# Performance work log

Measured on AMD Instinct MI355X. Metric: run time of the kernel, lower is better.

Reference implementation:

```python
import jax, jax.numpy as jnp
import numpy as np

N_NODES = 100000
N_EDGES = 1000000
D = 64
HID = 64
OUT = 64
N_CLS = 10
N_GRAPHS = 512
BN_EPS = 1e-5


def setup_inputs() -> dict:
    key = jax.random.key(0)
    ks = jax.random.split(key, 16)
    inp = {
        "x": jax.random.normal(ks[0], (N_NODES, D), dtype=jnp.float32),
        "edge_index": jax.random.randint(ks[1], (2, N_EDGES), 0, N_NODES, dtype=jnp.int32),
        "batch": jnp.sort(jax.random.randint(ks[2], (N_NODES,), 0, N_GRAPHS, dtype=jnp.int32)),
    }
    def lin(k, fi, fo):
        lim = 1.0 / np.sqrt(fi)
        kw, kb = jax.random.split(k)
        return (jax.random.uniform(kw, (fi, fo), minval=-lim, maxval=lim, dtype=jnp.float32),
                jax.random.uniform(kb, (fo,), minval=-lim, maxval=lim, dtype=jnp.float32))
    # conv0 MLP([64,64,64]) with BN after first linear
    inp["w0a"], inp["b0a"] = lin(ks[3], D, HID)
    inp["g0"] = jnp.ones((HID,), jnp.float32); inp["be0"] = jnp.zeros((HID,), jnp.float32)
    inp["m0"] = jnp.zeros((HID,), jnp.float32); inp["v0"] = jnp.ones((HID,), jnp.float32)
    inp["w0b"], inp["b0b"] = lin(ks[4], HID, HID)
    # conv1 MLP([64,64,64])
    inp["w1a"], inp["b1a"] = lin(ks[5], HID, HID)
    inp["g1"] = jnp.ones((HID,), jnp.float32); inp["be1"] = jnp.zeros((HID,), jnp.float32)
    inp["m1"] = jnp.zeros((HID,), jnp.float32); inp["v1"] = jnp.ones((HID,), jnp.float32)
    inp["w1b"], inp["b1b"] = lin(ks[6], HID, OUT)
    # classifier
    inp["wc"], inp["bc"] = lin(ks[7], OUT, N_CLS)
    return inp


def _bn_eval(h, g, b, m, v):
    return (h - m) * jax.lax.rsqrt(v + BN_EPS) * g + b


def _mlp(h, wa, ba, g, be, m, v, wb, bb):
    # Linear -> BN -> ReLU -> (dropout eval=identity) -> Linear
    h = h @ wa + ba
    h = jax.nn.relu(_bn_eval(h, g, be, m, v))
    return h @ wb + bb


def _gin_conv(h, src, dst, wa, ba, g, be, m, v, wb, bb):
    # GINConv eps=0: mlp(x + sum_{j->i} x_j), messages scatter-added at dst
    agg = jax.ops.segment_sum(h[src], dst, num_segments=N_NODES)
    return _mlp(h + agg, wa, ba, g, be, m, v, wb, bb)


def reference(x, edge_index, batch,
              w0a, b0a, g0, be0, m0, v0, w0b, b0b,
              w1a, b1a, g1, be1, m1, v1, w1b, b1b,
              wc, bc):
    src, dst = edge_index[0], edge_index[1]
    h = _gin_conv(x, src, dst, w0a, b0a, g0, be0, m0, v0, w0b, b0b)
    h = jax.nn.relu(h)  # dropout is identity in eval
    h = _gin_conv(h, src, dst, w1a, b1a, g1, be1, m1, v1, w1b, b1b)
    # global mean pool over batch indices
    sums = jax.ops.segment_sum(h, batch, num_segments=N_GRAPHS)
    cnts = jax.ops.segment_sum(jnp.ones((h.shape[0],), h.dtype), batch, num_segments=N_GRAPHS)
    pooled = sums / jnp.maximum(cnts, 1.0)[:, None]
    return pooled @ wc + bc
```

## Files before the change

### kernel.cpp

```cpp
#include <hip/hip_runtime.h>

#define N_NODES 100000
#define N_EDGES 1000000
#define N_GRAPHS 512
#define N_CLS 10
#define BN_EPS 1e-5f

#define SCAN_NB 200
#define NTILES2 3125

typedef _Float16 half8 __attribute__((ext_vector_type(8)));
typedef _Float16 half4v __attribute__((ext_vector_type(4)));
typedef float floatx4 __attribute__((ext_vector_type(4)));

__global__ __launch_bounds__(256) void prep_kernel(
    const float* __restrict__ x, _Float16* __restrict__ xh,
    const int* __restrict__ batch, const int* __restrict__ dstI,
    int* __restrict__ deg, int* __restrict__ rank,
    const float* __restrict__ w0a, const float* __restrict__ b0a,
    const float* __restrict__ g0, const float* __restrict__ be0,
    const float* __restrict__ m0, const float* __restrict__ v0,
    const float* __restrict__ w0b,
    const float* __restrict__ w1a, const float* __restrict__ b1a,
    const float* __restrict__ g1, const float* __restrict__ be1,
    const float* __restrict__ m1, const float* __restrict__ v1,
    const float* __restrict__ w1b,
    int* __restrict__ gstart,
    _Float16* __restrict__ wHi, _Float16* __restrict__ wLo,
    float* __restrict__ b1p0, float* __restrict__ b1p1) {
    const int gid = blockIdx.x * 256 + threadIdx.x;

    if (gid < 1600000) {
        float4 v = ((const float4*)x)[gid];
        half4v h = {(_Float16)v.x, (_Float16)v.y, (_Float16)v.z, (_Float16)v.w};
        ((half4v*)xh)[gid] = h;
    }

    if (gid < N_EDGES)
        rank[gid] = atomicAdd(&deg[dstI[gid]], 1);

    if (gid <= N_NODES) {
        int bcur = (gid < N_NODES) ? batch[gid] : N_GRAPHS;
        int bprev = (gid > 0) ? batch[gid - 1] : -1;
        for (int g = bprev + 1; g <= bcur; ++g) gstart[g] = gid;
    }

    if (gid < 16384) {
        const int e = gid & 4095, mat = gid >> 12;
        const int jj = e & 7, lane = (e >> 3) & 63, c = (e >> 9) & 3, k0 = (e >> 11) & 1;
        const int k = k0 * 32 + (lane >> 4) * 8 + jj;
        const int col = c * 16 + (lane & 15);
        float val;
        if (mat == 0)      val = w0a[k * 64 + col] * (rsqrtf(v0[col] + BN_EPS) * g0[col]);
        else if (mat == 1) val = w0b[k * 64 + col];
        else if (mat == 2) val = w1a[k * 64 + col] * (rsqrtf(v1[col] + BN_EPS) * g1[col]);
        else               val = w1b[k * 64 + col];
        _Float16 hi = (_Float16)val;
        wHi[gid] = hi;
        wLo[gid] = (_Float16)(val - (float)hi);
    }

    if (gid >= 16384 && gid < 16512) {
        int t = gid - 16384;
        if (t < 64) {
            float s = rsqrtf(v0[t] + BN_EPS) * g0[t];
            b1p0[t] = (b0a[t] - m0[t]) * s + be0[t];
        } else {
            t -= 64;
            float s = rsqrtf(v1[t] + BN_EPS) * g1[t];
            b1p1[t] = (b1a[t] - m1[t]) * s + be1[t];
        }
    }
}

__global__ __launch_bounds__(256) void scanA_kernel(const int* __restrict__ deg,
                                                    int* __restrict__ bsum) {
    __shared__ int sh[256];
    const int base = blockIdx.x * 512;
    const int t = threadIdx.x;
    int a = 0, b = 0;
    if (base + t < N_NODES) a = deg[base + t];
    if (base + 256 + t < N_NODES) b = deg[base + 256 + t];
    sh[t] = a + b;
    __syncthreads();
#pragma unroll
    for (int off = 128; off > 0; off >>= 1) {
        if (t < off) sh[t] += sh[t + off];
        __syncthreads();
    }
    if (t == 0) bsum[blockIdx.x] = sh[0];
}

__global__ __launch_bounds__(256) void scanC_kernel(const int* __restrict__ deg,
                                                    const int* __restrict__ bsum,
                                                    int* __restrict__ rowptr) {
    __shared__ int sh[256];
    __shared__ int sboff[256];
    const int base = blockIdx.x * 512;
    const int t = threadIdx.x;

    const int bv = (t < SCAN_NB) ? bsum[t] : 0;
    sboff[t] = bv;

    const int i0 = base + 2 * t, i1 = i0 + 1;
    const int d0 = (i0 < N_NODES) ? deg[i0] : 0;
    const int d1 = (i1 < N_NODES) ? deg[i1] : 0;
    const int p = d0 + d1;
    sh[t] = p;
    __syncthreads();
#pragma unroll
    for (int off = 1; off < 256; off <<= 1) {
        int u = (t >= off) ? sh[t - off] : 0;
        int ub = (t >= off) ? sboff[t - off] : 0;
        __syncthreads();
        sh[t] += u;
        sboff[t] += ub;
        __syncthreads();
    }
    const int myoff = (blockIdx.x == 0) ? 0 : sboff[blockIdx.x - 1];
    const int excl = myoff + sh[t] - p;
    if (i0 < N_NODES) rowptr[i0] = excl;
    if (i1 < N_NODES) rowptr[i1] = excl + d0;
    if (blockIdx.x == 0 && t == 0) rowptr[N_NODES] = N_EDGES;
}

__global__ __launch_bounds__(256) void fill_kernel(const int* __restrict__ srcI,
                                                   const int* __restrict__ dstI,
                                                   const int* __restrict__ rank,
                                                   const int* __restrict__ rowptr,
                                                   int* __restrict__ sortedSrc) {
    int e = blockIdx.x * 256 + threadIdx.x;
    if (e >= N_EDGES) return;
    sortedSrc[rowptr[dstI[e]] + rank[e]] = srcI[e];
}

__device__ __forceinline__ void idx_stage(const int* __restrict__ srcList, int rpv,
                                          int mq, int nodeSel, int slotSel, int& idxOwn) {
    const int rr0 = __shfl(rpv, mq * 4 + nodeSel, 64);
    const int rr1 = __shfl(rpv, mq * 4 + nodeSel + 1, 64);
    const int c = rr1 - rr0;
    const int e0 = (c > 0) ? min(slotSel, c - 1) : 0;
    int pos = rr0 + e0;
    pos = min(pos, N_EDGES - 1);
    idxOwn = srcList[pos];
}

__device__ __forceinline__ void rows_stage(const _Float16* __restrict__ in, int rpv,
                                           int mq, int strip0, int eoff, int lf,
                                           int idxOwn, half4v (&vT)[4][4], half4v (&sS)[4]) {
    const int m0 = mq * 4;
#pragma unroll
    for (int i = 0; i < 4; ++i) {
        sS[i] = (half4v){0, 0, 0, 0};
        if (eoff == 0)
            sS[i] = *(const half4v*)(in + (size_t)(strip0 + m0 + i) * 64 + lf * 4);
    }
#pragma unroll
    for (int i = 0; i < 4; ++i) {
        const int rr0 = __builtin_amdgcn_readlane(rpv, m0 + i);
        const int rr1 = __builtin_amdgcn_readlane(rpv, m0 + i + 1);
        const int cI = rr1 - rr0;
        const int g = (min(cI, 16) + 3) >> 2;
#pragma unroll
        for (int k = 0; k < 4; ++k) {
            vT[i][k] = (half4v){0, 0, 0, 0};
            if (k < g) {
                const int id = __shfl(idxOwn, i * 16 + 4 * k + eoff, 64);
                vT[i][k] = *(const half4v*)(in + (size_t)id * 64 + lf * 4);
            }
        }
    }
}

__device__ __forceinline__ void consume_stage(const _Float16* __restrict__ in,
                                              const int* __restrict__ srcList, int rpv,
                                              int mq, int eoff, int lf, int j,
                                              const half4v (&vT)[4][4], const half4v (&sS)[4],
                                              _Float16* aggH, _Float16* aggL) {
    const int m0 = mq * 4;
#pragma unroll
    for (int i = 0; i < 4; ++i) {
        const int rr0 = __builtin_amdgcn_readlane(rpv, m0 + i);
        const int rr1 = __builtin_amdgcn_readlane(rpv, m0 + i + 1);
        const int cI = rr1 - rr0;
        float aR[4] = {0.f, 0.f, 0.f, 0.f};
#pragma unroll
        for (int k = 0; k < 4; ++k) {
            if (4 * k + eoff < cI) {
                aR[0] += (float)vT[i][k].x; aR[1] += (float)vT[i][k].y;
                aR[2] += (float)vT[i][k].z; aR[3] += (float)vT[i][k].w;
            }
        }
        for (int eb = 16; eb < cI; eb += 16) {
#pragma unroll
            for (int k = 0; k < 4; ++k) {
                const int e_ = eb + 4 * k + eoff;
                if (e_ < cI) {
                    const int id = srcList[rr0 + e_];
                    half4v t = *(const half4v*)(in + (size_t)id * 64 + lf * 4);
                    aR[0] += (float)t.x; aR[1] += (float)t.y;
                    aR[2] += (float)t.z; aR[3] += (float)t.w;
                }
            }
        }
        if (eoff == 0) {
            aR[0] += (float)sS[i].x; aR[1] += (float)sS[i].y;
            aR[2] += (float)sS[i].z; aR[3] += (float)sS[i].w;
        }
#pragma unroll
        for (int q = 0; q < 4; ++q) {
            aR[q] += __shfl_xor(aR[q], 16, 64);
            aR[q] += __shfl_xor(aR[q], 32, 64);
        }
        if (j < 16) {
            half4v hi, lo;
#pragma unroll
            for (int q = 0; q < 4; ++q) {
                hi[q] = (_Float16)aR[q];
                lo[q] = (_Float16)(aR[q] - (float)hi[q]);
            }
            *(half4v*)(aggH + (m0 + i) * 72 + 4 * j) = hi;
            *(half4v*)(aggL + (m0 + i) * 72 + 4 * j) = lo;
        }
    }
}

#define SBAR() __builtin_amdgcn_sched_barrier(0)

template <int POOL>
__global__ __launch_bounds__(128, 4) void conv_mfma(
    const _Float16* __restrict__ in, const int* __restrict__ rowptr,
    const int* __restrict__ srcList,
    const _Float16* __restrict__ wH1, const _Float16* __restrict__ wL1,
    const _Float16* __restrict__ wH2, const _Float16* __restrict__ wL2,
    const float* __restrict__ b1, const float* __restrict__ b2,
    _Float16* __restrict__ out, const int* __restrict__ batch,
    float* __restrict__ pooled) {
    __shared__ __align__(16) _Float16 scratch[2][2304];
    __shared__ float pooledLoc[8 * 64];
    __shared__ int bIds[32];
    __shared__ int maxSlot;

    const int tid = threadIdx.x;
    const int j = tid & 63, wv = tid >> 6;
    const int eoff = j >> 4;
    const int lf = j & 15;
    const int base = blockIdx.x * 32;
    const int strip0 = base + wv * 16;

    if (POOL) {
#pragma unroll
        for (int q = 0; q < 4; ++q) pooledLoc[tid + q * 128] = 0.f;
        if (tid == 0) maxSlot = 0;
        if (j < 16) bIds[wv * 16 + j] = batch[strip0 + j];
    }

    const int rpv = rowptr[strip0 + min(j, 16)];

    _Float16* aggH = scratch[wv];
    _Float16* aggL = scratch[wv] + 1152;

    {
        int idxA, idxB, idxC;
        half4v vA[4][4], vB[4][4], sA[4], sB[4];

        idx_stage(srcList, rpv, 0, eoff, lf, idxA);
        idx_stage(srcList, rpv, 1, eoff, lf, idxB);
        SBAR();
        rows_stage(in, rpv, 0, strip0, eoff, lf, idxA, vA, sA);
        SBAR();
        idx_stage(srcList, rpv, 2, eoff, lf, idxC);
        SBAR();
        rows_stage(in, rpv, 1, strip0, eoff, lf, idxB, vB, sB);
        SBAR();
        consume_stage(in, srcList, rpv, 0, eoff, lf, j, vA, sA, aggH, aggL);
        SBAR();
        idx_stage(srcList, rpv, 3, eoff, lf, idxA);
        SBAR();
        rows_stage(in, rpv, 2, strip0, eoff, lf, idxC, vA, sA);
        SBAR();
        consume_stage(in, srcList, rpv, 1, eoff, lf, j, vB, sB, aggH, aggL);
        SBAR();
        rows_stage(in, rpv, 3, strip0, eoff, lf, idxA, vB, sB);
        SBAR();
        consume_stage(in, srcList, rpv, 2, eoff, lf, j, vA, sA, aggH, aggL);
        SBAR();
        consume_stage(in, srcList, rpv, 3, eoff, lf, j, vB, sB, aggH, aggL);
    }

    const int l15 = j & 15, quad = j >> 4;
    const floatx4 vzero = {0.f, 0.f, 0.f, 0.f};

    floatx4 acc[4] = {vzero, vzero, vzero, vzero};
    {
        const _Float16* aH0 = aggH + l15 * 72 + quad * 8;
        const _Float16* aL0 = aggL + l15 * 72 + quad * 8;
#pragma unroll
        for (int k0 = 0; k0 < 2; ++k0) {
            half8 aH = *(const half8*)(aH0 + k0 * 32);
            half8 aL = *(const half8*)(aL0 + k0 * 32);
#pragma unroll
            for (int c = 0; c < 4; ++c) {
                const int fo = ((k0 * 4 + c) * 64 + j) * 8;
                half8 bH = *(const half8*)(wH1 + fo);
                half8 bL = *(const half8*)(wL1 + fo);
                acc[c] = __builtin_amdgcn_mfma_f32_16x16x32_f16(aH, bH, acc[c], 0, 0, 0);
                acc[c] = __builtin_amdgcn_mfma_f32_16x16x32_f16(aL, bH, acc[c], 0, 0, 0);
                acc[c] = __builtin_amdgcn_mfma_f32_16x16x32_f16(aH, bL, acc[c], 0, 0, 0);
            }
        }
    }
    _Float16* hH = aggH;
    _Float16* hL = aggL;
#pragma unroll
    for (int c = 0; c < 4; ++c) {
        const float bv = b1[c * 16 + l15];
#pragma unroll
        for (int r = 0; r < 4; ++r) {
            const int row = quad * 4 + r, col = c * 16 + l15;
            float v = acc[c][r] + bv;
            v = fmaxf(v, 0.f);
            const _Float16 hi = (_Float16)v;
            hH[row * 72 + col] = hi;
            hL[row * 72 + col] = (_Float16)(v - (float)hi);
        }
    }

    floatx4 acc2[4] = {vzero, vzero, vzero, vzero};
    {
        const _Float16* aH0 = hH + l15 * 72 + quad * 8;
        const _Float16* aL0 = hL + l15 * 72 + quad * 8;
#pragma unroll
        for (int k0 = 0; k0 < 2; ++k0) {
            half8 aH = *(const half8*)(aH0 + k0 * 32);
            half8 aL = *(const half8*)(aL0 + k0 * 32);
#pragma unroll
            for (int c = 0; c < 4; ++c) {
                const int fo = ((k0 * 4 + c) * 64 + j) * 8;
                half8 bH = *(const half8*)(wH2 + fo);
                half8 bL = *(const half8*)(wL2 + fo);
                acc2[c] = __builtin_amdgcn_mfma_f32_16x16x32_f16(aH, bH, acc2[c], 0, 0, 0);
                acc2[c] = __builtin_amdgcn_mfma_f32_16x16x32_f16(aL, bH, acc2[c], 0, 0, 0);
                acc2[c] = __builtin_amdgcn_mfma_f32_16x16x32_f16(aH, bL, acc2[c], 0, 0, 0);
            }
        }
    }

    if (!POOL) {
#pragma unroll
        for (int c = 0; c < 4; ++c) {
            const float bv = b2[c * 16 + l15];
#pragma unroll
            for (int r = 0; r < 4; ++r) {
                const int node = strip0 + quad * 4 + r;
                out[(size_t)node * 64 + c * 16 + l15] =
                    (_Float16)fmaxf(acc2[c][r] + bv, 0.f);
            }
        }
    } else {
        float* oT = (float*)scratch[wv];
#pragma unroll
        for (int c = 0; c < 4; ++c) {
            const float bv = b2[c * 16 + l15];
#pragma unroll
            for (int r = 0; r < 4; ++r)
                oT[(quad * 4 + r) * 66 + c * 16 + l15] = acc2[c][r] + bv;
        }
        __syncthreads();
        const int b0 = bIds[0];
        int curB = -1;
        float accv = 0.f;
        for (int r = 0; r < 16; ++r) {
            const int b = bIds[wv * 16 + r];
            const float v = oT[r * 66 + j];
            if (b != curB) {
                if (curB >= 0) {
                    const int s = curB - b0;
                    if (s >= 0 && s < 8) {
                        atomicAdd(&pooledLoc[s * 64 + j], accv);
                        if (j == 0) atomicMax(&maxSlot, s);
                    } else {
                        atomicAdd(&pooled[curB * 64 + j], accv);
                    }
                }
                curB = b;
                accv = v;
            } else {
                accv += v;
            }
        }
        {
            const int s = curB - b0;
            if (s >= 0 && s < 8) {
                atomicAdd(&pooledLoc[s * 64 + j], accv);
                if (j == 0) atomicMax(&maxSlot, s);
            } else {
                atomicAdd(&pooled[curB * 64 + j], accv);
            }
        }
        __syncthreads();
        const int ns = maxSlot + 1;
        for (int s = wv; s < ns; s += 2)
            atomicAdd(&pooled[(b0 + s) * 64 + j], pooledLoc[s * 64 + j]);
    }
}

__global__ __launch_bounds__(64) void classifier_kernel(const float* __restrict__ pooled,
                                                        const int* __restrict__ gstart,
                                                        const float* __restrict__ wc,
                                                        const float* __restrict__ bc,
                                                        float* __restrict__ out) {
    const int g = blockIdx.x;
    const int j = threadIdx.x;
    const float c = fmaxf((float)(gstart[g + 1] - gstart[g]), 1.f);
    const float mean = pooled[g * 64 + j] / c;
#pragma unroll
    for (int cc = 0; cc < N_CLS; ++cc) {
        float p = mean * wc[j * N_CLS + cc];
#pragma unroll
        for (int off = 32; off > 0; off >>= 1) p += __shfl_down(p, off, 64);
        if (j == 0) out[g * N_CLS + cc] = p + bc[cc];
    }
}


extern "C" void kernel_launch(void* const* d_in, const int* in_sizes, int n_in,
                              void* d_out, int out_size, void* d_ws, size_t ws_size,
                              hipStream_t stream) {
    const float* x   = (const float*)d_in[0];
    const int*   ei  = (const int*)d_in[1];
    const int* batch = (const int*)d_in[2];
    const float* w0a = (const float*)d_in[3];
    const float* b0a = (const float*)d_in[4];
    const float* g0  = (const float*)d_in[5];
    const float* be0 = (const float*)d_in[6];
    const float* m0  = (const float*)d_in[7];
    const float* v0  = (const float*)d_in[8];
    const float* w0b = (const float*)d_in[9];
    const float* b0b = (const float*)d_in[10];
    const float* w1a = (const float*)d_in[11];
    const float* b1a = (const float*)d_in[12];
    const float* g1  = (const float*)d_in[13];
    const float* be1 = (const float*)d_in[14];
    const float* m1  = (const float*)d_in[15];
    const float* v1  = (const float*)d_in[16];
    const float* w1b = (const float*)d_in[17];
    const float* b1b = (const float*)d_in[18];
    const float* wc  = (const float*)d_in[19];
    const float* bc  = (const float*)d_in[20];
    float* out = (float*)d_out;

    const int* srcI = ei;
    const int* dstI = ei + N_EDGES;

    int* ws = (int*)d_ws;
    int*      deg       = ws;
    int*      bsum      = ws + 100000;
    float*    pooled    = (float*)(ws + 100404);
    int*      rowptr    = ws + 133172;
    int*      rank      = ws + 233176;
    int*      sortedSrc = ws + 1233176;
    _Float16* xh        = (_Float16*)(ws + 2233176);
    _Float16* h1        = (_Float16*)(ws + 5433176);
    float*    b1p0      = (float*)(ws + 8633176);
    float*    b1p1      = (float*)(ws + 8633240);
    int*      gstart    = ws + 8633304;
    _Float16* wHi       = (_Float16*)(ws + 8633820);
    _Float16* wLo       = (_Float16*)(ws + 8642012);

    (void)hipMemsetAsync((void*)deg, 0, 133172 * sizeof(int), stream);
    prep_kernel<<<6250, 256, 0, stream>>>(x, xh, batch, dstI, deg, rank,
                                          w0a, b0a, g0, be0, m0, v0, w0b,
                                          w1a, b1a, g1, be1, m1, v1, w1b,
                                          gstart, wHi, wLo, b1p0, b1p1);

    scanA_kernel<<<SCAN_NB, 256, 0, stream>>>(deg, bsum);
    scanC_kernel<<<SCAN_NB, 256, 0, stream>>>(deg, bsum, rowptr);
    fill_kernel<<<(N_EDGES + 255) / 256, 256, 0, stream>>>(srcI, dstI, rank, rowptr, sortedSrc);

    conv_mfma<0><<<NTILES2, 128, 0, stream>>>(xh, rowptr, sortedSrc,
                                              wHi, wLo, wHi + 4096, wLo + 4096,
                                              b1p0, b0b, h1, nullptr, nullptr);

    conv_mfma<1><<<NTILES2, 128, 0, stream>>>(h1, rowptr, sortedSrc,
                                              wHi + 8192, wLo + 8192, wHi + 12288, wLo + 12288,
                                              b1p1, b1b, nullptr, batch, pooled);

    classifier_kernel<<<N_GRAPHS, 64, 0, stream>>>(pooled, gstart, wc, bc, out);
}
```

Before: 279.1 us.

## Swizzle LDS tiles and drop block-level pooling staging in conv kernel

Replaces the padded stride-72 LDS layout for the aggregation and hidden tiles with an unpadded stride-64 XOR swizzle, shrinking shared memory per block. In the pooling variant it removes the shared-memory pooled staging, the block barriers and the atomicMax. Each wave now reads batch ids through readlane and issues global atomics per run of equal graph ids. The smaller LDS footprint and fewer barriers may raise occupancy, at the cost of more global atomics on the pooled array.

```diff
diff --git a/kernel.cpp b/kernel.cpp
--- a/kernel.cpp
+++ b/kernel.cpp
@@ -134,6 +134,10 @@
     sortedSrc[rowptr[dstI[e]] + rank[e]] = srcI[e];
 }
 
+__device__ __forceinline__ int swz(int row, int col) {
+    return row * 64 + (col ^ ((row & 7) << 3));
+}
+
 __device__ __forceinline__ void idx_stage(const int* __restrict__ srcList, int rpv,
                                           int mq, int nodeSel, int slotSel, int& idxOwn) {
     const int rr0 = __shfl(rpv, mq * 4 + nodeSel, 64);
@@ -219,8 +223,9 @@
                 hi[q] = (_Float16)aR[q];
                 lo[q] = (_Float16)(aR[q] - (float)hi[q]);
             }
-            *(half4v*)(aggH + (m0 + i) * 72 + 4 * j) = hi;
-            *(half4v*)(aggL + (m0 + i) * 72 + 4 * j) = lo;
+            const int idx = swz(m0 + i, 4 * j);
+            *(half4v*)(aggH + idx) = hi;
+            *(half4v*)(aggL + idx) = lo;
         }
     }
 }
@@ -236,10 +241,7 @@
     const float* __restrict__ b1, const float* __restrict__ b2,
     _Float16* __restrict__ out, const int* __restrict__ batch,
     float* __restrict__ pooled) {
-    __shared__ __align__(16) _Float16 scratch[2][2304];
-    __shared__ float pooledLoc[8 * 64];
-    __shared__ int bIds[32];
-    __shared__ int maxSlot;
+    __shared__ __align__(16) unsigned char scratch[2][4096];
 
     const int tid = threadIdx.x;
     const int j = tid & 63, wv = tid >> 6;
@@ -248,17 +250,13 @@
     const int base = blockIdx.x * 32;
     const int strip0 = base + wv * 16;
 
-    if (POOL) {
-#pragma unroll
-        for (int q = 0; q < 4; ++q) pooledLoc[tid + q * 128] = 0.f;
-        if (tid == 0) maxSlot = 0;
-        if (j < 16) bIds[wv * 16 + j] = batch[strip0 + j];
-    }
+    int bb = 0;
+    if (POOL) bb = batch[strip0 + min(j, 15)];
 
     const int rpv = rowptr[strip0 + min(j, 16)];
 
-    _Float16* aggH = scratch[wv];
-    _Float16* aggL = scratch[wv] + 1152;
+    _Float16* aggH = (_Float16*)scratch[wv];
+    _Float16* aggL = aggH + 1024;
 
     {
         int idxA, idxB, idxC;
@@ -293,12 +291,11 @@
 
     floatx4 acc[4] = {vzero, vzero, vzero, vzero};
     {
-        const _Float16* aH0 = aggH + l15 * 72 + quad * 8;
-        const _Float16* aL0 = aggL + l15 * 72 + quad * 8;
 #pragma unroll
         for (int k0 = 0; k0 < 2; ++k0) {
-            half8 aH = *(const half8*)(aH0 + k0 * 32);
-            half8 aL = *(const half8*)(aL0 + k0 * 32);
+            const int aidx = swz(l15, quad * 8 + k0 * 32);
+            half8 aH = *(const half8*)(aggH + aidx);
+            half8 aL = *(const half8*)(aggL + aidx);
 #pragma unroll
             for (int c = 0; c < 4; ++c) {
                 const int fo = ((k0 * 4 + c) * 64 + j) * 8;
@@ -317,23 +314,22 @@
         const float bv = b1[c * 16 + l15];
 #pragma unroll
         for (int r = 0; r < 4; ++r) {
-            const int row = quad * 4 + r, col = c * 16 + l15;
+            const int idx = swz(quad * 4 + r, c * 16 + l15);
             float v = acc[c][r] + bv;
             v = fmaxf(v, 0.f);
             const _Float16 hi = (_Float16)v;
-            hH[row * 72 + col] = hi;
-            hL[row * 72 + col] = (_Float16)(v - (float)hi);
+            hH[idx] = hi;
+            hL[idx] = (_Float16)(v - (float)hi);
         }
     }
 
     floatx4 acc2[4] = {vzero, vzero, vzero, vzero};
     {
-        const _Float16* aH0 = hH + l15 * 72 + quad * 8;
-        const _Float16* aL0 = hL + l15 * 72 + quad * 8;
 #pragma unroll
         for (int k0 = 0; k0 < 2; ++k0) {
-            half8 aH = *(const half8*)(aH0 + k0 * 32);
-            half8 aL = *(const half8*)(aL0 + k0 * 32);
+            const int aidx = swz(l15, quad * 8 + k0 * 32);
+            half8 aH = *(const half8*)(hH + aidx);
+            half8 aL = *(const half8*)(hL + aidx);
 #pragma unroll
             for (int c = 0; c < 4; ++c) {
                 const int fo = ((k0 * 4 + c) * 64 + j) * 8;
@@ -364,44 +360,24 @@
             const float bv = b2[c * 16 + l15];
 #pragma unroll
             for (int r = 0; r < 4; ++r)
-                oT[(quad * 4 + r) * 66 + c * 16 + l15] = acc2[c][r] + bv;
-        }
-        __syncthreads();
-        const int b0 = bIds[0];
+                oT[(quad * 4 + r) * 64 + c * 16 + l15] = acc2[c][r] + bv;
+        }
+        __builtin_amdgcn_s_waitcnt(0);
         int curB = -1;
         float accv = 0.f;
+#pragma unroll
         for (int r = 0; r < 16; ++r) {
-            const int b = bIds[wv * 16 + r];
-            const float v = oT[r * 66 + j];
+            const int b = __builtin_amdgcn_readlane(bb, r);
+            const float v = oT[r * 64 + j];
             if (b != curB) {
-                if (curB >= 0) {
-                    const int s = curB - b0;
-                    if (s >= 0 && s < 8) {
-                        atomicAdd(&pooledLoc[s * 64 + j], accv);
-                        if (j == 0) atomicMax(&maxSlot, s);
-                    } else {
-                        atomicAdd(&pooled[curB * 64 + j], accv);
-                    }
-                }
+                if (curB >= 0) atomicAdd(&pooled[curB * 64 + j], accv);
                 curB = b;
                 accv = v;
             } else {
                 accv += v;
             }
         }
-        {
-            const int s = curB - b0;
-            if (s >= 0 && s < 8) {
-                atomicAdd(&pooledLoc[s * 64 + j], accv);
-                if (j == 0) atomicMax(&maxSlot, s);
-            } else {
-                atomicAdd(&pooled[curB * 64 + j], accv);
-            }
-        }
-        __syncthreads();
-        const int ns = maxSlot + 1;
-        for (int s = wv; s < ns; s += 2)
-            atomicAdd(&pooled[(b0 + s) * 64 + j], pooledLoc[s * 64 + j]);
+        atomicAdd(&pooled[curB * 64 + j], accv);
     }
 }
 
```

Result: no change. 279.1 us (-0.0%).
